# Kernel optimization log

Measured on AMD Instinct MI355X. Metric: run time of the kernel, lower is better.

The kernel has to match this reference:

```python
import jax, jax.numpy as jnp
import numpy as np

IMG_H, IMG_W = 900, 1600
NUM_CLASSES = 10
NUM_CAMS = 6

# pcdet boxes_to_corners_3d corner template (unit box, centered)
CORNER_TEMPLATE = jnp.array(
    [[1, 1, -1], [1, -1, -1], [-1, -1, -1], [-1, 1, -1],
     [1, 1, 1], [1, -1, 1], [-1, -1, 1], [-1, 1, 1]], dtype=jnp.float32) * 0.5


def boxes_to_corners_3d(boxes):
    # boxes: [N,7] = (x,y,z,dx,dy,dz,heading) -> [N,8,3]
    dims = boxes[:, 3:6]
    corners = dims[:, None, :] * CORNER_TEMPLATE  # [N,8,3]
    yaw = boxes[:, 6]
    c, s = jnp.cos(yaw), jnp.sin(yaw)
    z = jnp.zeros_like(c)
    o = jnp.ones_like(c)
    # rotate_points_along_z: points @ [[c,s,0],[-s,c,0],[0,0,1]]
    rot = jnp.stack([c, s, z, -s, c, z, z, z, o], axis=-1).reshape(-1, 3, 3)
    corners = jnp.einsum('nkj,njm->nkm', corners, rot)
    return corners + boxes[:, None, 0:3]


def box_iou(a, b):
    # a: [M,4], b: [K,4] xyxy -> [M,K]
    lt = jnp.maximum(a[:, None, :2], b[None, :, :2])
    rb = jnp.minimum(a[:, None, 2:], b[None, :, 2:])
    wh = jnp.clip(rb - lt, 0.0)
    inter = wh[..., 0] * wh[..., 1]
    area_a = (a[:, 2] - a[:, 0]) * (a[:, 3] - a[:, 1])
    area_b = (b[:, 2] - b[:, 0]) * (b[:, 3] - b[:, 1])
    union = area_a[:, None] + area_b[None, :] - inter
    return jnp.where(union > 0, inter / union, 0.0)


def _project_boxes(pred_boxes, img_aug_matrix, lidar_aug_matrix, lidar2image):
    # batch index 0 (B=1); returns proj [6,N,4] and valid [6,N]
    N = pred_boxes.shape[0]
    corners = boxes_to_corners_3d(pred_boxes).reshape(-1, 3)  # [N*8,3]
    la = lidar_aug_matrix[0]
    pts = corners - la[:3, 3]
    pts = jnp.linalg.inv(la[:3, :3]) @ pts.T  # [3, N*8]
    l2i = lidar2image[0]
    cc = l2i[:, :3, :3] @ pts + l2i[:, :3, 3][:, :, None]  # [6,3,N*8]
    zc = jnp.clip(cc[:, 2, :], 1e-5, 1e5)
    xy = cc[:, :2, :] / zc[:, None, :]
    cc = jnp.concatenate([xy, zc[:, None, :]], axis=1)
    ia = img_aug_matrix[0]
    cc = ia[:, :3, :3] @ cc + ia[:, :3, 3][:, :, None]
    pix = jnp.transpose(cc[:, :2, :], (0, 2, 1))  # [6, N*8, 2]
    # .long() truncation (non-differentiable in original)
    pix = jax.lax.stop_gradient(pix).astype(jnp.int32)
    px = jnp.clip(pix[..., 0], 0, IMG_W)
    py = jnp.clip(pix[..., 1], 0, IMG_H)
    pix = jnp.stack([px, py], -1).reshape(NUM_CAMS, N, 8, 2).astype(pred_boxes.dtype)
    xy1 = pix.min(axis=2)  # [6,N,2]
    xy2 = pix.max(axis=2)
    valid = jnp.all((xy2 - xy1) > 0, axis=-1)  # [6,N]
    proj = jnp.concatenate([xy1, xy2], axis=-1)  # [6,N,4]
    return proj, valid


def setup_inputs() -> dict:
    rng = np.random.default_rng(0)
    N, M = 4096, 6144
    xy = rng.uniform(-40, 40, (N, 2))
    zc = rng.uniform(-1, 1, (N, 1))
    dims = rng.uniform(1.0, 4.0, (N, 3))
    yaw = rng.uniform(0, 2 * np.pi, (N, 1))
    pred_boxes = np.concatenate([xy, zc, dims, yaw], axis=1).astype(np.float32)
    # 6 cameras: pinhole intrinsics + yaw-spaced extrinsics
    K = np.array([[1000., 0., 800.], [0., 1000., 450.], [0., 0., 1.]])
    l2i = np.zeros((1, NUM_CAMS, 4, 4), np.float32)
    for ci, ang in enumerate(np.linspace(0, 2 * np.pi, NUM_CAMS, endpoint=False)):
        fwd = np.array([np.cos(ang), np.sin(ang), 0.])
        right = np.array([np.sin(ang), -np.cos(ang), 0.])
        down = np.array([0., 0., -1.])
        R = np.stack([right, down, fwd], 0)
        l2i[0, ci, :3, :3] = K @ R
        l2i[0, ci, 3, 3] = 1.0
    img_aug_matrix = np.tile(np.eye(4, dtype=np.float32), (1, NUM_CAMS, 1, 1))
    lidar_aug_matrix = np.eye(4, dtype=np.float32)[None]
    cx = rng.uniform(0, IMG_W, M)
    cy = rng.uniform(0, IMG_H, M)
    w = rng.uniform(20, 300, M)
    h = rng.uniform(20, 300, M)
    det_boxes = np.stack([np.clip(cx - w / 2, 0, IMG_W), np.clip(cy - h / 2, 0, IMG_H),
                          np.clip(cx + w / 2, 0, IMG_W), np.clip(cy + h / 2, 0, IMG_H)], 1).astype(np.float32)
    det_labels = rng.integers(1, NUM_CLASSES + 1, M).astype(np.int32)
    det_scores = rng.uniform(0.05, 1.0, M).astype(np.float32)
    det_batch_idx = np.zeros(M, np.int32)
    det_cam_idx = (np.arange(M) % NUM_CAMS).astype(np.int32)
    return {
        'pred_boxes': jnp.asarray(pred_boxes),
        'img_aug_matrix': jnp.asarray(img_aug_matrix),
        'lidar_aug_matrix': jnp.asarray(lidar_aug_matrix),
        'lidar2image': jnp.asarray(l2i),
        'det_boxes': jnp.asarray(det_boxes),
        'det_labels': jnp.asarray(det_labels),
        'det_scores': jnp.asarray(det_scores),
        'det_batch_idx': jnp.asarray(det_batch_idx),
        'det_cam_idx': jnp.asarray(det_cam_idx),
    }


def reference(pred_boxes, img_aug_matrix, lidar_aug_matrix, lidar2image,
              det_boxes, det_labels, det_scores, det_batch_idx, det_cam_idx):
    proj, valid = _project_boxes(pred_boxes, img_aug_matrix, lidar_aug_matrix, lidar2image)
    label_matrix = jax.nn.one_hot(det_labels - 1, NUM_CLASSES, dtype=det_scores.dtype) * det_scores[:, None]
    probs_sum = jnp.zeros((pred_boxes.shape[0], NUM_CLASSES), dtype=det_scores.dtype)
    for c in range(NUM_CAMS):
        mask = ((det_cam_idx == c) & (det_batch_idx == 0)).astype(det_boxes.dtype)
        iou = box_iou(det_boxes, proj[c]) * mask[:, None]  # [M,N]
        probs_sum = probs_sum + (iou.T @ label_matrix) * valid[c][:, None]  # [N,10]
    denom = 1e-5 + valid.astype(probs_sum.dtype).sum(axis=0)
    box_probs_mean = probs_sum / denom[:, None]
    pred_scores = jnp.nan_to_num(jnp.max(box_probs_mean, axis=-1), nan=0.0)
    pred_labels = jnp.argmax(box_probs_mean, axis=-1) + 1
    return pred_labels, pred_scores
```

## Files before the change

kernel.cpp:

```cpp
#include <hip/hip_runtime.h>
#include <cstdint>
#include <climits>

#pragma clang fp contract(off)

#define NCAM 6
#define NCLS 10
#define IMGW 1600
#define IMGH 900

__device__ __forceinline__ int sat_f2i(float f) {
    if (f != f) return 0;
    if (f >= 2147483648.0f) return INT_MAX;
    if (f <= -2147483648.0f) return INT_MIN;
    return (int)f;
}

__global__ __launch_bounds__(256) void fused_kernel(
        const float* __restrict__ boxes,
        const float* __restrict__ ia,
        const float* __restrict__ la,
        const float* __restrict__ l2i,
        const float4* __restrict__ det_boxes,
        const int*    __restrict__ det_labels,
        const float*  __restrict__ det_scores,
        const int*    __restrict__ det_batch,
        const int*    __restrict__ det_cam,
        float* __restrict__ out,
        int N, int M) {
    int n = blockIdx.x;
    int tid = threadIdx.x;
    if (n >= N) return;

    __shared__ float sP[NCAM][6];
    __shared__ float red[NCLS][256];

    if (tid < NCAM) {
        int cam = tid;
        float bx = boxes[n*7+0], by = boxes[n*7+1], bz = boxes[n*7+2];
        float dx = boxes[n*7+3], dy = boxes[n*7+4], dz = boxes[n*7+5];
        float yaw = boxes[n*7+6];
        float c = (float)cos((double)yaw);
        float s = (float)sin((double)yaw);

        float a00=la[0],a01=la[1],a02=la[2],t0=la[3];
        float a10=la[4],a11=la[5],a12=la[6],t1=la[7];
        float a20=la[8],a21=la[9],a22=la[10],t2=la[11];
        float det = a00*(a11*a22-a12*a21) - a01*(a10*a22-a12*a20) + a02*(a10*a21-a11*a20);
        float id = 1.0f/det;
        float r00=(a11*a22-a12*a21)*id, r01=(a02*a21-a01*a22)*id, r02=(a01*a12-a02*a11)*id;
        float r10=(a12*a20-a10*a22)*id, r11=(a00*a22-a02*a20)*id, r12=(a02*a10-a00*a12)*id;
        float r20=(a10*a21-a11*a20)*id, r21=(a01*a20-a00*a21)*id, r22=(a00*a11-a01*a10)*id;

        const float* L = l2i + cam*16;
        const float* A = ia  + cam*16;
        int minx = INT_MAX, miny = INT_MAX, maxx = INT_MIN, maxy = INT_MIN;
        #pragma unroll
        for (int k = 0; k < 8; k++) {
            float sx = ((k==0||k==1||k==4||k==5) ?  0.5f : -0.5f) * dx;
            float sy = ((k==0||k==3||k==4||k==7) ?  0.5f : -0.5f) * dy;
            float sz = ((k>=4)                   ?  0.5f : -0.5f) * dz;
            float cx = sx*c - sy*s + bx;
            float cy = sx*s + sy*c + by;
            float cz = sz + bz;
            float ux = cx - t0, uy = cy - t1, uz = cz - t2;
            float PX = r00*ux + r01*uy + r02*uz;
            float PY = r10*ux + r11*uy + r12*uz;
            float PZ = r20*ux + r21*uy + r22*uz;

            float u = L[0]*PX + L[1]*PY + L[2]*PZ  + L[3];
            float v = L[4]*PX + L[5]*PY + L[6]*PZ  + L[7];
            float w = L[8]*PX + L[9]*PY + L[10]*PZ + L[11];
            float zc = fminf(fmaxf(w, 1e-5f), 100000.0f);
            float x = u / zc, y = v / zc;
            float xx = A[0]*x + A[1]*y + A[2]*zc + A[3];
            float yy = A[4]*x + A[5]*y + A[6]*zc + A[7];
            int pxi = sat_f2i(xx); pxi = min(max(pxi, 0), IMGW);
            int pyi = sat_f2i(yy); pyi = min(max(pyi, 0), IMGH);
            minx = min(minx, pxi); maxx = max(maxx, pxi);
            miny = min(miny, pyi); maxy = max(maxy, pyi);
        }
        float x1 = (float)minx, y1 = (float)miny, x2 = (float)maxx, y2 = (float)maxy;
        float validf = ((x2 - x1) > 0.0f && (y2 - y1) > 0.0f) ? 1.0f : 0.0f;
        sP[cam][0] = x1; sP[cam][1] = y1; sP[cam][2] = x2; sP[cam][3] = y2;
        sP[cam][4] = (x2 - x1) * (y2 - y1);
        sP[cam][5] = validf;
    }
    __syncthreads();

    float probs[NCLS];
    #pragma unroll
    for (int k = 0; k < NCLS; k++) probs[k] = 0.0f;

    for (int m = tid; m < M; m += 256) {
        float4 b = det_boxes[m];
        int cam = det_cam[m];
        int bi  = det_batch[m];
        int cls = det_labels[m] - 1;
        float sc = det_scores[m];
        if (bi == 0 && cam >= 0 && cam < NCAM && cls >= 0 && cls < NCLS) {
            const float* P = sP[cam];
            float ltx = fmaxf(b.x, P[0]);
            float lty = fmaxf(b.y, P[1]);
            float rbx = fminf(b.z, P[2]);
            float rby = fminf(b.w, P[3]);
            float iw = fmaxf(rbx - ltx, 0.0f);
            float ih = fmaxf(rby - lty, 0.0f);
            float inter = iw * ih;
            float area_a = (b.z - b.x) * (b.w - b.y);
            float uni = area_a + P[4] - inter;
            float iou = (uni > 0.0f) ? (inter / uni) : 0.0f;
            float w = iou * P[5] * sc;
            #pragma unroll
            for (int k = 0; k < NCLS; k++) probs[k] += (k == cls) ? w : 0.0f;
        }
    }

    #pragma unroll
    for (int k = 0; k < NCLS; k++) red[k][tid] = probs[k];
    __syncthreads();
    for (int s = 128; s > 0; s >>= 1) {
        if (tid < s) {
            #pragma unroll
            for (int k = 0; k < NCLS; k++) red[k][tid] += red[k][tid + s];
        }
        __syncthreads();
    }
    if (tid == 0) {
        float nv = 0.0f;
        for (int c2 = 0; c2 < NCAM; c2++) nv += sP[c2][5];
        float denom = 1e-5f + nv;
        float best = -1.0f; int bestk = 0;
        #pragma unroll
        for (int k = 0; k < NCLS; k++) {
            float v = red[k][0] / denom;
            if (v > best) { best = v; bestk = k; }
        }
        out[n]     = (float)(bestk + 1);
        out[N + n] = best;
    }
}

extern "C" void kernel_launch(void* const* d_in, const int* in_sizes, int n_in,
                              void* d_out, int out_size, void* d_ws, size_t ws_size,
                              hipStream_t stream) {
    const float*  pred_boxes = (const float*)d_in[0];
    const float*  ia         = (const float*)d_in[1];
    const float*  la         = (const float*)d_in[2];
    const float*  l2i        = (const float*)d_in[3];
    const float4* det_boxes  = (const float4*)d_in[4];
    const int*    det_labels = (const int*)d_in[5];
    const float*  det_scores = (const float*)d_in[6];
    const int*    det_batch  = (const int*)d_in[7];
    const int*    det_cam    = (const int*)d_in[8];
    float* out = (float*)d_out;

    int N = in_sizes[0] / 7;
    int M = in_sizes[4] / 4;

    fused_kernel<<<N, 256, 0, stream>>>(pred_boxes, ia, la, l2i,
                                        det_boxes, det_labels, det_scores,
                                        det_batch, det_cam, out, N, M);
}
```

Baseline: 127.4 us.

## Bucket detections by camera and class, then compute per-box IoU sums

The single fused kernel, which used one block per predicted box and scanned every detection, is replaced by three kernels. A prep kernel projects boxes with one thread per box and compacts detections into per-(camera, class) slabs using ballot prefix sums. A main kernel assigns one thread per box and iterates only over its bucket, with detections staged in shared memory. A reduce kernel then sums across buckets and takes the argmax. This removes the redundant full scan of M per box and the one-hot class accumulation. In exchange it adds launch overhead, a fixed bucket capacity of 1024 that would overflow on larger buckets, and an approximate division.

```diff
diff --git a/kernel.cpp b/kernel.cpp
--- a/kernel.cpp
+++ b/kernel.cpp
@@ -6,8 +6,11 @@
 
 #define NCAM 6
 #define NCLS 10
+#define NKEY 60
 #define IMGW 1600
 #define IMGH 900
+#define CAP 1024
+#define STAGE 512
 
 __device__ __forceinline__ int sat_f2i(float f) {
     if (f != f) return 0;
@@ -16,27 +19,25 @@
     return (int)f;
 }
 
-__global__ __launch_bounds__(256) void fused_kernel(
-        const float* __restrict__ boxes,
-        const float* __restrict__ ia,
-        const float* __restrict__ la,
-        const float* __restrict__ l2i,
+__global__ __launch_bounds__(256) void prep_kernel(
+        const float*  __restrict__ boxes,
+        const float*  __restrict__ ia,
+        const float*  __restrict__ la,
+        const float*  __restrict__ l2i,
         const float4* __restrict__ det_boxes,
         const int*    __restrict__ det_labels,
         const float*  __restrict__ det_scores,
         const int*    __restrict__ det_batch,
         const int*    __restrict__ det_cam,
-        float* __restrict__ out,
-        int N, int M) {
-    int n = blockIdx.x;
+        float* __restrict__ projW,
+        float* __restrict__ slab,
+        int*   __restrict__ cnt,
+        int N, int M, int PB) {
     int tid = threadIdx.x;
-    if (n >= N) return;
-
-    __shared__ float sP[NCAM][6];
-    __shared__ float red[NCLS][256];
-
-    if (tid < NCAM) {
-        int cam = tid;
+
+    if ((int)blockIdx.x < PB) {
+        int n = blockIdx.x * 256 + tid;
+        if (n >= N) return;
         float bx = boxes[n*7+0], by = boxes[n*7+1], bz = boxes[n*7+2];
         float dx = boxes[n*7+3], dy = boxes[n*7+4], dz = boxes[n*7+5];
         float yaw = boxes[n*7+6];
@@ -52,9 +53,7 @@
         float r10=(a12*a20-a10*a22)*id, r11=(a00*a22-a02*a20)*id, r12=(a02*a10-a00*a12)*id;
         float r20=(a10*a21-a11*a20)*id, r21=(a01*a20-a00*a21)*id, r22=(a00*a11-a01*a10)*id;
 
-        const float* L = l2i + cam*16;
-        const float* A = ia  + cam*16;
-        int minx = INT_MAX, miny = INT_MAX, maxx = INT_MIN, maxy = INT_MIN;
+        float PX[8], PY[8], PZ[8];
         #pragma unroll
         for (int k = 0; k < 8; k++) {
             float sx = ((k==0||k==1||k==4||k==5) ?  0.5f : -0.5f) * dx;
@@ -64,81 +63,156 @@
             float cy = sx*s + sy*c + by;
             float cz = sz + bz;
             float ux = cx - t0, uy = cy - t1, uz = cz - t2;
-            float PX = r00*ux + r01*uy + r02*uz;
-            float PY = r10*ux + r11*uy + r12*uz;
-            float PZ = r20*ux + r21*uy + r22*uz;
-
-            float u = L[0]*PX + L[1]*PY + L[2]*PZ  + L[3];
-            float v = L[4]*PX + L[5]*PY + L[6]*PZ  + L[7];
-            float w = L[8]*PX + L[9]*PY + L[10]*PZ + L[11];
-            float zc = fminf(fmaxf(w, 1e-5f), 100000.0f);
-            float x = u / zc, y = v / zc;
-            float xx = A[0]*x + A[1]*y + A[2]*zc + A[3];
-            float yy = A[4]*x + A[5]*y + A[6]*zc + A[7];
-            int pxi = sat_f2i(xx); pxi = min(max(pxi, 0), IMGW);
-            int pyi = sat_f2i(yy); pyi = min(max(pyi, 0), IMGH);
-            minx = min(minx, pxi); maxx = max(maxx, pxi);
-            miny = min(miny, pyi); maxy = max(maxy, pyi);
-        }
-        float x1 = (float)minx, y1 = (float)miny, x2 = (float)maxx, y2 = (float)maxy;
-        float validf = ((x2 - x1) > 0.0f && (y2 - y1) > 0.0f) ? 1.0f : 0.0f;
-        sP[cam][0] = x1; sP[cam][1] = y1; sP[cam][2] = x2; sP[cam][3] = y2;
-        sP[cam][4] = (x2 - x1) * (y2 - y1);
-        sP[cam][5] = validf;
-    }
+            PX[k] = r00*ux + r01*uy + r02*uz;
+            PY[k] = r10*ux + r11*uy + r12*uz;
+            PZ[k] = r20*ux + r21*uy + r22*uz;
+        }
+        for (int cam = 0; cam < NCAM; cam++) {
+            const float* L = l2i + cam*16;
+            const float* A = ia  + cam*16;
+            int minx = INT_MAX, miny = INT_MAX, maxx = INT_MIN, maxy = INT_MIN;
+            #pragma unroll
+            for (int k = 0; k < 8; k++) {
+                float u = L[0]*PX[k] + L[1]*PY[k] + L[2]*PZ[k]  + L[3];
+                float v = L[4]*PX[k] + L[5]*PY[k] + L[6]*PZ[k]  + L[7];
+                float w = L[8]*PX[k] + L[9]*PY[k] + L[10]*PZ[k] + L[11];
+                float zc = fminf(fmaxf(w, 1e-5f), 100000.0f);
+                float x = u / zc, y = v / zc;
+                float xx = A[0]*x + A[1]*y + A[2]*zc + A[3];
+                float yy = A[4]*x + A[5]*y + A[6]*zc + A[7];
+                int pxi = sat_f2i(xx); pxi = min(max(pxi, 0), IMGW);
+                int pyi = sat_f2i(yy); pyi = min(max(pyi, 0), IMGH);
+                minx = min(minx, pxi); maxx = max(maxx, pxi);
+                miny = min(miny, pyi); maxy = max(maxy, pyi);
+            }
+            float x1 = (float)minx, y1 = (float)miny, x2 = (float)maxx, y2 = (float)maxy;
+            float validf = ((x2 - x1) > 0.0f && (y2 - y1) > 0.0f) ? 1.0f : 0.0f;
+            projW[(cam*6+0)*N + n] = x1;
+            projW[(cam*6+1)*N + n] = y1;
+            projW[(cam*6+2)*N + n] = x2;
+            projW[(cam*6+3)*N + n] = y2;
+            projW[(cam*6+4)*N + n] = (x2 - x1) * (y2 - y1);
+            projW[(cam*6+5)*N + n] = validf;
+        }
+        return;
+    }
+
+    int k = (int)blockIdx.x - PB;
+    int cam = k / NCLS, cls = k % NCLS;
+    __shared__ int wcnt[4];
+    __shared__ int running;
+    if (tid == 0) running = 0;
+    int lane = tid & 63, w = tid >> 6;
     __syncthreads();
 
-    float probs[NCLS];
-    #pragma unroll
-    for (int k = 0; k < NCLS; k++) probs[k] = 0.0f;
-
-    for (int m = tid; m < M; m += 256) {
-        float4 b = det_boxes[m];
-        int cam = det_cam[m];
-        int bi  = det_batch[m];
-        int cls = det_labels[m] - 1;
-        float sc = det_scores[m];
-        if (bi == 0 && cam >= 0 && cam < NCAM && cls >= 0 && cls < NCLS) {
-            const float* P = sP[cam];
-            float ltx = fmaxf(b.x, P[0]);
-            float lty = fmaxf(b.y, P[1]);
-            float rbx = fminf(b.z, P[2]);
-            float rby = fminf(b.w, P[3]);
-            float iw = fmaxf(rbx - ltx, 0.0f);
-            float ih = fmaxf(rby - lty, 0.0f);
-            float inter = iw * ih;
-            float area_a = (b.z - b.x) * (b.w - b.y);
-            float uni = area_a + P[4] - inter;
-            float iou = (uni > 0.0f) ? (inter / uni) : 0.0f;
-            float w = iou * P[5] * sc;
-            #pragma unroll
-            for (int k = 0; k < NCLS; k++) probs[k] += (k == cls) ? w : 0.0f;
-        }
-    }
-
-    #pragma unroll
-    for (int k = 0; k < NCLS; k++) red[k][tid] = probs[k];
+    for (int c = 0; c < M; c += 256) {
+        int m = c + tid;
+        bool pred = false;
+        if (m < M) {
+            int dc = det_cam[m], db = det_batch[m], dl = det_labels[m] - 1;
+            pred = (db == 0) && (dc == cam) && (dl == cls);
+        }
+        unsigned long long ball = __ballot(pred);
+        if (lane == 0) wcnt[w] = __popcll(ball);
+        __syncthreads();
+        int base = running;
+        int pre = 0;
+        #pragma unroll
+        for (int j = 0; j < 4; j++) pre += (j < w) ? wcnt[j] : 0;
+        int tot = wcnt[0] + wcnt[1] + wcnt[2] + wcnt[3];
+        if (pred) {
+            int pos = base + pre + __popcll(ball & ((1ull << lane) - 1ull));
+            float4 b = det_boxes[m];
+            float area = (b.z - b.x) * (b.w - b.y);
+            float4* o = (float4*)(slab + ((size_t)k * CAP + pos) * 8);
+            o[0] = b;
+            o[1] = make_float4(area, det_scores[m], 0.0f, 0.0f);
+        }
+        __syncthreads();
+        if (tid == 0) running += tot;
+    }
     __syncthreads();
-    for (int s = 128; s > 0; s >>= 1) {
-        if (tid < s) {
-            #pragma unroll
-            for (int k = 0; k < NCLS; k++) red[k][tid] += red[k][tid + s];
-        }
-        __syncthreads();
-    }
-    if (tid == 0) {
-        float nv = 0.0f;
-        for (int c2 = 0; c2 < NCAM; c2++) nv += sP[c2][5];
-        float denom = 1e-5f + nv;
-        float best = -1.0f; int bestk = 0;
+    if (tid == 0) cnt[k] = running;
+}
+
+__global__ __launch_bounds__(256) void main_kernel(
+        const float* __restrict__ projW,
+        const float* __restrict__ slab,
+        const int*   __restrict__ cnt,
+        float*       __restrict__ partial,
+        int N) {
+    int tid = threadIdx.x;
+    int k = blockIdx.y;
+    int cam = k / NCLS;
+    int box = blockIdx.x * 256 + tid;
+    __shared__ float4 sd[STAGE * 2];
+
+    int nk = cnt[k];
+    float Px1 = 0, Py1 = 0, Px2 = 0, Py2 = 0, Pa = 0, Pv = 0;
+    if (box < N) {
+        Px1 = projW[(cam*6+0)*N + box];
+        Py1 = projW[(cam*6+1)*N + box];
+        Px2 = projW[(cam*6+2)*N + box];
+        Py2 = projW[(cam*6+3)*N + box];
+        Pa  = projW[(cam*6+4)*N + box];
+        Pv  = projW[(cam*6+5)*N + box];
+    }
+    float acc = 0.0f;
+    const float4* gsl = (const float4*)slab;
+
+    for (int base = 0; base < nk; base += STAGE) {
+        int cc = min(STAGE, nk - base);
+        __syncthreads();
+        for (int i = tid; i < cc * 2; i += 256)
+            sd[i] = gsl[((size_t)k * CAP + base) * 2 + i];
+        __syncthreads();
+        if (box < N) {
+            for (int m = 0; m < cc; m++) {
+                float4 b = sd[2*m];
+                float4 q = sd[2*m+1];
+                float ltx = fmaxf(b.x, Px1);
+                float lty = fmaxf(b.y, Py1);
+                float rbx = fminf(b.z, Px2);
+                float rby = fminf(b.w, Py2);
+                float iw = fmaxf(rbx - ltx, 0.0f);
+                float ih = fmaxf(rby - lty, 0.0f);
+                float inter = iw * ih;
+                float uni = (q.x + Pa) - inter;
+                float r = __fdividef(inter, uni);
+                float iou = (uni > 0.0f) ? r : 0.0f;
+                acc += iou * q.y;
+            }
+        }
+    }
+    if (box < N) partial[(size_t)k * N + box] = acc * Pv;
+}
+
+__global__ __launch_bounds__(256) void reduce_kernel(
+        const float* __restrict__ partial,
+        const float* __restrict__ projW,
+        float* __restrict__ out, int N) {
+    int n = blockIdx.x * 256 + threadIdx.x;
+    if (n >= N) return;
+    float p[NCLS];
+    #pragma unroll
+    for (int c = 0; c < NCLS; c++) p[c] = 0.0f;
+    #pragma unroll
+    for (int cam = 0; cam < NCAM; cam++)
         #pragma unroll
-        for (int k = 0; k < NCLS; k++) {
-            float v = red[k][0] / denom;
-            if (v > best) { best = v; bestk = k; }
-        }
-        out[n]     = (float)(bestk + 1);
-        out[N + n] = best;
-    }
+        for (int c = 0; c < NCLS; c++)
+            p[c] += partial[(size_t)(cam * NCLS + c) * N + n];
+    float nv = 0.0f;
+    #pragma unroll
+    for (int cam = 0; cam < NCAM; cam++) nv += projW[(cam*6+5)*N + n];
+    float denom = 1e-5f + nv;
+    float best = -1e30f; int bk = 0;
+    #pragma unroll
+    for (int c = 0; c < NCLS; c++) {
+        float v = p[c] / denom;
+        if (v > best) { best = v; bk = c; }
+    }
+    out[n]     = (float)(bk + 1);
+    out[N + n] = best;
 }
 
 extern "C" void kernel_launch(void* const* d_in, const int* in_sizes, int n_in,
@@ -157,8 +231,21 @@
 
     int N = in_sizes[0] / 7;
     int M = in_sizes[4] / 4;
-
-    fused_kernel<<<N, 256, 0, stream>>>(pred_boxes, ia, la, l2i,
-                                        det_boxes, det_labels, det_scores,
-                                        det_batch, det_cam, out, N, M);
-}
+    int PB = (N + 255) / 256;
+
+    char* w = (char*)d_ws;
+    float* slab    = (float*)w;
+    size_t off = (size_t)NKEY * CAP * 8 * 4;
+    float* projW   = (float*)(w + off);
+    off += (size_t)36 * N * 4;
+    float* partial = (float*)(w + off);
+    off += (size_t)NKEY * N * 4;
+    int*   cnt     = (int*)(w + off);
+
+    prep_kernel<<<PB + NKEY, 256, 0, stream>>>(pred_boxes, ia, la, l2i,
+                                               det_boxes, det_labels, det_scores,
+                                               det_batch, det_cam,
+                                               projW, slab, cnt, N, M, PB);
+    main_kernel<<<dim3(PB, NKEY), 256, 0, stream>>>(projW, slab, cnt, partial, N);
+    reduce_kernel<<<PB, 256, 0, stream>>>(partial, projW, out, N);
+}
```

Measured after the change: 118.6 us. -7.0%, faster.
